# Kernel tuning notes

Measured on AMD Instinct MI355X. Metric: run time of the kernel, lower is better.

The kernel has to match this reference:

```python
import jax, jax.numpy as jnp
import numpy as np

N_EPOCH = 1000
LR = 1e-3      # torch.optim.Adam defaults
BETA1 = 0.9
BETA2 = 0.999
EPS = 1e-8


def setup_inputs() -> dict:
    key = jax.random.key(0)
    k1, k2 = jax.random.split(key)
    H = jax.random.normal(k1, (128, 2048), dtype=jnp.float32)        # test activations [n_test, d]
    H_train = jax.random.normal(k2, (2048, 2048), dtype=jnp.float32)  # corpus activations [n_train, d]
    return {"H": H, "H_train": H_train}


def reference(H, H_train):
    n_test, n_train = H.shape[0], H_train.shape[0]

    def loss_fn(P):
        W = jax.nn.softmax(P, axis=-1)              # [n_test, n_train]
        H_approx = W @ H_train                       # einsum ij,jk->ik
        return jnp.sum((H_approx - H) ** 2)

    grad_fn = jax.grad(loss_fn)

    P0 = jnp.zeros((n_test, n_train), dtype=H.dtype)
    m0 = jnp.zeros_like(P0)
    v0 = jnp.zeros_like(P0)

    def adam_step(carry, t):
        P, m, v = carry
        g = grad_fn(P)
        m = BETA1 * m + (1.0 - BETA1) * g
        v = BETA2 * v + (1.0 - BETA2) * (g * g)
        m_hat = m / (1.0 - BETA1 ** t)
        v_hat = v / (1.0 - BETA2 ** t)
        P = P - LR * m_hat / (jnp.sqrt(v_hat) + EPS)
        return (P, m, v), None

    steps = jnp.arange(1, N_EPOCH + 1, dtype=H.dtype)  # 1-based Adam step count
    (P, _, _), _ = jax.lax.scan(adam_step, (P0, m0, v0), steps)
    return jax.nn.softmax(P, axis=-1)
```

## Files before the change

### kernel.cpp

```cpp
#include <hip/hip_runtime.h>
#include <math.h>

#define DN 2048
#define NT 128

#define KS   16
#define KSL  128
#define KCH  32
#define CB   256
#define RB   32

constexpr float LR    = 1e-3f;
constexpr float BETA1 = 0.9f;
constexpr float BETA2 = 0.999f;
constexpr float EPSA  = 1e-8f;

__device__ __forceinline__ float f4get(const float4& v, int k) {
    return k == 0 ? v.x : (k == 1 ? v.y : (k == 2 ? v.z : v.w));
}

__global__ __launch_bounds__(256)
void wa_kernel(const float* __restrict__ W, const float* __restrict__ A,
               float* __restrict__ parts)
{
    __shared__ __align__(16) float At[KCH][CB];
    const int colb  = blockIdx.x * CB;
    const int rowb  = blockIdx.y * RB;
    const int kb    = blockIdx.z;
    const int kbase = kb * KSL;
    const int tx    = threadIdx.x;
    const int lane  = tx & 63;
    const int wid   = __builtin_amdgcn_readfirstlane(tx >> 6);
    const int row0  = rowb + wid * 8;

    const float* wbase = W + (size_t)row0 * DN + kbase;

    float4 acc[8];
    #pragma unroll
    for (int r = 0; r < 8; ++r) acc[r] = {0.f, 0.f, 0.f, 0.f};

    #pragma unroll 1
    for (int ch = 0; ch < KSL / KCH; ++ch) {
        __syncthreads();
        {
            const float* src = A + (size_t)(kbase + ch * KCH) * DN + colb;
            #pragma unroll
            for (int it = 0; it < 8; ++it) {
                const int f  = it * 256 + tx;
                const int kr = f >> 6;
                const int c4 = f & 63;
                *(float4*)&At[kr][c4 * 4] =
                    *(const float4*)&src[(size_t)kr * DN + c4 * 4];
            }
        }
        __syncthreads();

        #pragma unroll
        for (int kc = 0; kc < KCH / 4; ++kc) {
            float4 wv[8];
            #pragma unroll
            for (int r = 0; r < 8; ++r)
                wv[r] = *(const float4*)(wbase + (size_t)r * DN + ch * KCH + kc * 4);
            #pragma unroll
            for (int kk = 0; kk < 4; ++kk) {
                const float4 av = *(const float4*)&At[4 * kc + kk][lane * 4];
                #pragma unroll
                for (int r = 0; r < 8; ++r) {
                    const float wk = f4get(wv[r], kk);
                    acc[r].x += wk * av.x; acc[r].y += wk * av.y;
                    acc[r].z += wk * av.z; acc[r].w += wk * av.w;
                }
            }
        }
    }

    float* op = parts + (size_t)kb * (NT * DN);
    #pragma unroll
    for (int r = 0; r < 8; ++r)
        *(float4*)&op[(size_t)(row0 + r) * DN + colb + lane * 4] = acc[r];
}

__global__ __launch_bounds__(512)
void bpart_kernel(const float* __restrict__ L, const float* __restrict__ R,
                  float* __restrict__ out_parts)
{
    __shared__ __align__(16) float Ws[128][36];
    __shared__ __align__(16) float At[32][36];
    const int j0    = blockIdx.x * 32;
    const int kbase = blockIdx.y * 512;
    const int tx = threadIdx.x;
    const int cg = tx & 7;
    const int rg = tx >> 3;
    float4 acc0 = {0.f, 0.f, 0.f, 0.f};
    float4 acc1 = {0.f, 0.f, 0.f, 0.f};

    for (int s = 0; s < 16; ++s) {
        const int k0 = kbase + s * 32;
        {
            int idx = tx;
            #pragma unroll
            for (int rr = 0; rr < 2; ++rr) {
                const int row = idx >> 3, f = idx & 7;
                const float4 wv = *(const float4*)&L[row * DN + k0 + 4 * f];
                *(float4*)&Ws[row][4 * f] = wv;
                idx += 512;
            }
            if (tx < 256) {
                const int c = tx >> 3, f = tx & 7;
                const float4 av = *(const float4*)&R[(size_t)(j0 + c) * DN + k0 + 4 * f];
                At[4 * f + 0][c] = av.x;
                At[4 * f + 1][c] = av.y;
                At[4 * f + 2][c] = av.z;
                At[4 * f + 3][c] = av.w;
            }
        }
        __syncthreads();
        #pragma unroll
        for (int kq = 0; kq < 8; ++kq) {
            const float4 w0 = *(const float4*)&Ws[rg][4 * kq];
            const float4 w1 = *(const float4*)&Ws[rg + 64][4 * kq];
            #pragma unroll
            for (int kk = 0; kk < 4; ++kk) {
                const float4 av = *(const float4*)&At[4 * kq + kk][4 * cg];
                const float wa = f4get(w0, kk);
                const float wb = f4get(w1, kk);
                acc0.x += wa * av.x; acc0.y += wa * av.y;
                acc0.z += wa * av.z; acc0.w += wa * av.w;
                acc1.x += wb * av.x; acc1.y += wb * av.y;
                acc1.z += wb * av.z; acc1.w += wb * av.w;
            }
        }
        __syncthreads();
    }
    float* op = out_parts + (size_t)blockIdx.y * (NT * DN);
    *(float4*)&op[rg * DN + j0 + 4 * cg] = acc0;
    *(float4*)&op[(rg + 64) * DN + j0 + 4 * cg] = acc1;
}

__global__ __launch_bounds__(256)
void gram_kernel(const float* __restrict__ Ht, float* __restrict__ A)
{
    __shared__ __align__(16) float Ti[64][36];
    __shared__ __align__(16) float Tj[64][36];
    const int i0 = blockIdx.x * 64, j0 = blockIdx.y * 64;
    const int tx = threadIdx.x;
    const int ti = tx & 15;
    const int tj = tx >> 4;
    float4 acc[4];
    #pragma unroll
    for (int a = 0; a < 4; ++a) acc[a] = {0.f, 0.f, 0.f, 0.f};

    for (int s = 0; s < 64; ++s) {
        const int k0 = s * 32;
        {
            int idx = tx;
            #pragma unroll
            for (int rr = 0; rr < 2; ++rr) {
                const int row = idx >> 3, f = idx & 7;
                *(float4*)&Ti[row][4 * f] = *(const float4*)&Ht[(size_t)(i0 + row) * DN + k0 + 4 * f];
                *(float4*)&Tj[row][4 * f] = *(const float4*)&Ht[(size_t)(j0 + row) * DN + k0 + 4 * f];
                idx += 256;
            }
        }
        __syncthreads();
        #pragma unroll
        for (int kq = 0; kq < 8; ++kq) {
            float4 iv[4], jv[4];
            #pragma unroll
            for (int a = 0; a < 4; ++a) iv[a] = *(const float4*)&Ti[ti + 16 * a][4 * kq];
            #pragma unroll
            for (int b = 0; b < 4; ++b) jv[b] = *(const float4*)&Tj[4 * tj + b][4 * kq];
            #pragma unroll
            for (int kk = 0; kk < 4; ++kk) {
                #pragma unroll
                for (int a = 0; a < 4; ++a) {
                    const float wa = f4get(iv[a], kk);
                    acc[a].x += wa * f4get(jv[0], kk);
                    acc[a].y += wa * f4get(jv[1], kk);
                    acc[a].z += wa * f4get(jv[2], kk);
                    acc[a].w += wa * f4get(jv[3], kk);
                }
            }
        }
        __syncthreads();
    }
    #pragma unroll
    for (int a = 0; a < 4; ++a)
        *(float4*)&A[(size_t)(i0 + ti + 16 * a) * DN + j0 + 4 * tj] = acc[a];
}

__global__ void sumB_kernel(const float* __restrict__ parts, float* __restrict__ Bm)
{
    const int idx = (blockIdx.x * 256 + threadIdx.x) * 4;
    float4 a = *(const float4*)&parts[idx];
    const float4 b = *(const float4*)&parts[(size_t)NT * DN + idx];
    const float4 c = *(const float4*)&parts[(size_t)2 * NT * DN + idx];
    const float4 d = *(const float4*)&parts[(size_t)3 * NT * DN + idx];
    a.x += b.x; a.x += c.x; a.x += d.x;
    a.y += b.y; a.y += c.y; a.y += d.y;
    a.z += b.z; a.z += c.z; a.z += d.z;
    a.w += b.w; a.w += c.w; a.w += d.w;
    *(float4*)&Bm[idx] = a;
}

__global__ void init_kernel(float* __restrict__ P, float* __restrict__ M,
                            float* __restrict__ V, float* __restrict__ W)
{
    const int idx = (blockIdx.x * 256 + threadIdx.x) * 4;
    const float4 z = {0.f, 0.f, 0.f, 0.f};
    const float u = 1.f / (float)DN;
    const float4 uu = {u, u, u, u};
    *(float4*)&P[idx] = z;
    *(float4*)&M[idx] = z;
    *(float4*)&V[idx] = z;
    *(float4*)&W[idx] = uu;
}

__device__ __forceinline__ float blk_sum(float x) {
    #pragma unroll
    for (int o = 32; o > 0; o >>= 1) x += __shfl_down(x, o);
    __shared__ float r[8];
    const int tx = threadIdx.x;
    if ((tx & 63) == 0) r[tx >> 6] = x;
    __syncthreads();
    x = ((r[0] + r[1]) + (r[2] + r[3])) + ((r[4] + r[5]) + (r[6] + r[7]));
    __syncthreads();
    return x;
}

__device__ __forceinline__ float blk_max(float x) {
    #pragma unroll
    for (int o = 32; o > 0; o >>= 1) x = fmaxf(x, __shfl_down(x, o));
    __shared__ float r[8];
    const int tx = threadIdx.x;
    if ((tx & 63) == 0) r[tx >> 6] = x;
    __syncthreads();
    x = fmaxf(fmaxf(fmaxf(r[0], r[1]), fmaxf(r[2], r[3])),
              fmaxf(fmaxf(r[4], r[5]), fmaxf(r[6], r[7])));
    __syncthreads();
    return x;
}

__global__ __launch_bounds__(512)
void adam_kernel(const float* __restrict__ parts, const float* __restrict__ Bm,
                 float* __restrict__ W, float* __restrict__ P,
                 float* __restrict__ M, float* __restrict__ V,
                 const float bc1, const float bc2)
{
    const int i = blockIdx.x;
    const int tx = threadIdx.x;
    const int base = i * DN + tx * 4;

    float4 s = {0.f, 0.f, 0.f, 0.f};
    #pragma unroll
    for (int p = 0; p < KS; ++p) {
        const float4 x = *(const float4*)&parts[(size_t)p * (NT * DN) + base];
        s.x += x.x; s.y += x.y; s.z += x.z; s.w += x.w;
    }
    const float4 b = *(const float4*)&Bm[base];
    float G4[4] = { 2.f * (s.x - b.x), 2.f * (s.y - b.y),
                    2.f * (s.z - b.z), 2.f * (s.w - b.w) };

    float W4[4], P4[4], M4[4], V4[4], E4[4];
    *(float4*)&W4[0] = *(const float4*)&W[base];

    float sp = 0.f;
    #pragma unroll
    for (int e = 0; e < 4; ++e) sp += W4[e] * G4[e];
    const float srow = blk_sum(sp);

    *(float4*)&P4[0] = *(const float4*)&P[base];
    *(float4*)&M4[0] = *(const float4*)&M[base];
    *(float4*)&V4[0] = *(const float4*)&V[base];

    float mx = -1e30f;
    #pragma unroll
    for (int e = 0; e < 4; ++e) {
        const float g  = W4[e] * (G4[e] - srow);
        const float m_ = BETA1 * M4[e] + (1.f - BETA1) * g;
        const float v_ = BETA2 * V4[e] + (1.f - BETA2) * g * g;
        M4[e] = m_; V4[e] = v_;
        const float mh = m_ * bc1;
        const float vh = v_ * bc2;
        const float pn = P4[e] - LR * mh / (sqrtf(vh) + EPSA);
        P4[e] = pn;
        mx = fmaxf(mx, pn);
    }
    mx = blk_max(mx);

    float es = 0.f;
    #pragma unroll
    for (int e = 0; e < 4; ++e) { E4[e] = expf(P4[e] - mx); es += E4[e]; }
    const float sig = blk_sum(es);
    #pragma unroll
    for (int e = 0; e < 4; ++e) W4[e] = E4[e] / sig;

    *(float4*)&W[base] = *(const float4*)&W4[0];
    *(float4*)&P[base] = *(const float4*)&P4[0];
    *(float4*)&M[base] = *(const float4*)&M4[0];
    *(float4*)&V[base] = *(const float4*)&V4[0];
}

extern "C" void kernel_launch(void* const* d_in, const int* in_sizes, int n_in,
                              void* d_out, int out_size, void* d_ws, size_t ws_size,
                              hipStream_t stream)
{
    const float* H  = (const float*)d_in[0];
    const float* Ht = (const float*)d_in[1];

    float* ws = (float*)d_ws;
    float* A     = ws;
    float* Bm    = A  + (size_t)DN * DN;
    float* P     = Bm + (size_t)NT * DN;
    float* M     = P  + (size_t)NT * DN;
    float* V     = M  + (size_t)NT * DN;
    float* W     = V  + (size_t)NT * DN;
    float* parts = W  + (size_t)NT * DN;

    gram_kernel<<<dim3(32, 32), 256, 0, stream>>>(Ht, A);
    bpart_kernel<<<dim3(64, 4), 512, 0, stream>>>(H, Ht, parts);
    sumB_kernel<<<256, 256, 0, stream>>>(parts, Bm);
    init_kernel<<<256, 256, 0, stream>>>(P, M, V, W);

    double b1t = 1.0, b2t = 1.0;
    for (int t = 1; t <= 1000; ++t) {
        b1t *= 0.9; b2t *= 0.999;
        wa_kernel<<<dim3(DN / CB, NT / RB, KS), 256, 0, stream>>>(W, A, parts);
        const float bc1 = (float)(1.0 / (1.0 - b1t));
        const float bc2 = (float)(1.0 / (1.0 - b2t));
        adam_kernel<<<NT, 512, 0, stream>>>(parts, Bm, W, P, M, V, bc1, bc2);
    }

    hipMemcpyAsync(d_out, W, (size_t)NT * DN * sizeof(float),
                   hipMemcpyDeviceToDevice, stream);
}
```

Measured before the change: 28.14 ms.

## Double-buffer A tile in wa_kernel and retile to 512 threads with 8x2 outputs

Reworks the per-step W·A GEMM kernel so the shared-memory A chunk is double-buffered, with the next chunk prefetched while the current one is consumed, and one barrier per chunk. Tile shape changes to 64 rows x 128 columns with 16-deep K chunks and 512 threads, each thread computing 8x2 outputs instead of 8x4. This is meant to hide global-load latency and raise occupancy. In exchange each thread does less work per W load, so W is re-read more often relative to the FMAs.

```diff
diff --git a/kernel.cpp b/kernel.cpp
--- a/kernel.cpp
+++ b/kernel.cpp
@@ -6,9 +6,9 @@
 
 #define KS   16
 #define KSL  128
-#define KCH  32
-#define CB   256
-#define RB   32
+#define KCH  16
+#define CB   128
+#define RB   64
 
 constexpr float LR    = 1e-3f;
 constexpr float BETA1 = 0.9f;
@@ -19,11 +19,11 @@
     return k == 0 ? v.x : (k == 1 ? v.y : (k == 2 ? v.z : v.w));
 }
 
-__global__ __launch_bounds__(256)
+__global__ __launch_bounds__(512, 4)
 void wa_kernel(const float* __restrict__ W, const float* __restrict__ A,
                float* __restrict__ parts)
 {
-    __shared__ __align__(16) float At[KCH][CB];
+    __shared__ __align__(16) float At[2][KCH][CB];
     const int colb  = blockIdx.x * CB;
     const int rowb  = blockIdx.y * RB;
     const int kb    = blockIdx.z;
@@ -35,26 +35,28 @@
 
     const float* wbase = W + (size_t)row0 * DN + kbase;
 
-    float4 acc[8];
-    #pragma unroll
-    for (int r = 0; r < 8; ++r) acc[r] = {0.f, 0.f, 0.f, 0.f};
+    const int s_kr = tx >> 5;
+    const int s_c4 = tx & 31;
+
+    float2 acc[8];
+    #pragma unroll
+    for (int r = 0; r < 8; ++r) acc[r] = {0.f, 0.f};
+
+    {
+        const float* src = A + (size_t)(kbase + 0 * KCH) * DN + colb;
+        *(float4*)&At[0][s_kr][s_c4 * 4] =
+            *(const float4*)&src[(size_t)s_kr * DN + s_c4 * 4];
+    }
+    __syncthreads();
 
     #pragma unroll 1
     for (int ch = 0; ch < KSL / KCH; ++ch) {
-        __syncthreads();
-        {
-            const float* src = A + (size_t)(kbase + ch * KCH) * DN + colb;
-            #pragma unroll
-            for (int it = 0; it < 8; ++it) {
-                const int f  = it * 256 + tx;
-                const int kr = f >> 6;
-                const int c4 = f & 63;
-                *(float4*)&At[kr][c4 * 4] =
-                    *(const float4*)&src[(size_t)kr * DN + c4 * 4];
-            }
-        }
-        __syncthreads();
-
+        if (ch + 1 < KSL / KCH) {
+            const float* src = A + (size_t)(kbase + (ch + 1) * KCH) * DN + colb;
+            *(float4*)&At[(ch + 1) & 1][s_kr][s_c4 * 4] =
+                *(const float4*)&src[(size_t)s_kr * DN + s_c4 * 4];
+        }
+        const int buf = ch & 1;
         #pragma unroll
         for (int kc = 0; kc < KCH / 4; ++kc) {
             float4 wv[8];
@@ -63,21 +65,22 @@
                 wv[r] = *(const float4*)(wbase + (size_t)r * DN + ch * KCH + kc * 4);
             #pragma unroll
             for (int kk = 0; kk < 4; ++kk) {
-                const float4 av = *(const float4*)&At[4 * kc + kk][lane * 4];
+                const float2 av = *(const float2*)&At[buf][4 * kc + kk][lane * 2];
                 #pragma unroll
                 for (int r = 0; r < 8; ++r) {
                     const float wk = f4get(wv[r], kk);
-                    acc[r].x += wk * av.x; acc[r].y += wk * av.y;
-                    acc[r].z += wk * av.z; acc[r].w += wk * av.w;
+                    acc[r].x += wk * av.x;
+                    acc[r].y += wk * av.y;
                 }
             }
         }
-    }
-
-    float* op = parts + (size_t)kb * (NT * DN);
+        __syncthreads();
+    }
+
+    float* op = parts + (size_t)kb * (NT * DN) + colb + lane * 2;
     #pragma unroll
     for (int r = 0; r < 8; ++r)
-        *(float4*)&op[(size_t)(row0 + r) * DN + colb + lane * 4] = acc[r];
+        *(float2*)&op[(size_t)(row0 + r) * DN] = acc[r];
 }
 
 __global__ __launch_bounds__(512)
@@ -325,7 +328,7 @@
     double b1t = 1.0, b2t = 1.0;
     for (int t = 1; t <= 1000; ++t) {
         b1t *= 0.9; b2t *= 0.999;
-        wa_kernel<<<dim3(DN / CB, NT / RB, KS), 256, 0, stream>>>(W, A, parts);
+        wa_kernel<<<dim3(DN / CB, NT / RB, KS), 512, 0, stream>>>(W, A, parts);
         const float bc1 = (float)(1.0 / (1.0 - b1t));
         const float bc2 = (float)(1.0 / (1.0 - b2t));
         adam_kernel<<<NT, 512, 0, stream>>>(parts, Bm, W, P, M, V, bc1, bc2);
```

New measurement: 30.21 ms. 1.07x slower.

## Retile W·A GEMM with shared-memory W tile, 8x8 register blocking, double buffering

Applied to the files above, without the earlier changes.

Rewrites the per-step W·A product so each block stages both a transposed W tile and an A tile in padded, double-buffered shared memory. Each thread computes an 8x8 output block, which raises arithmetic intensity over the old scheme where every thread read W straight from global memory. The next chunk's loads are overlapped with compute on the current chunk. The split-K factor rises from 16 to 32, which doubles the partial-sum buffer written here and then reduced by the Adam kernel. It also adds a launch-bounds occupancy hint.

```diff
diff --git a/kernel.cpp b/kernel.cpp
--- a/kernel.cpp
+++ b/kernel.cpp
@@ -4,11 +4,11 @@
 #define DN 2048
 #define NT 128
 
-#define KS   16
-#define KSL  128
-#define KCH  32
-#define CB   256
-#define RB   32
+#define KS   32
+#define KSL  64
+#define KC   16
+#define CB   128
+#define PADW 132
 
 constexpr float LR    = 1e-3f;
 constexpr float BETA1 = 0.9f;
@@ -19,72 +19,102 @@
     return k == 0 ? v.x : (k == 1 ? v.y : (k == 2 ? v.z : v.w));
 }
 
-__global__ __launch_bounds__(256)
+__global__ __launch_bounds__(256, 2)
 void wa_kernel(const float* __restrict__ W, const float* __restrict__ A,
                float* __restrict__ parts)
 {
-    __shared__ __align__(16) float At[KCH][CB];
-    const int colb  = blockIdx.x * CB;
-    const int rowb  = blockIdx.y * RB;
-    const int kb    = blockIdx.z;
-    const int kbase = kb * KSL;
-    const int tx    = threadIdx.x;
-    const int lane  = tx & 63;
-    const int wid   = __builtin_amdgcn_readfirstlane(tx >> 6);
-    const int row0  = rowb + wid * 8;
-
-    const float* wbase = W + (size_t)row0 * DN + kbase;
-
-    float4 acc[8];
-    #pragma unroll
-    for (int r = 0; r < 8; ++r) acc[r] = {0.f, 0.f, 0.f, 0.f};
+    __shared__ __align__(16) float Ws[2][KC][PADW];
+    __shared__ __align__(16) float As[2][KC][PADW];
+    const int c0 = blockIdx.x * CB;
+    const int kb = blockIdx.y;
+    const int k0 = kb * KSL;
+    const int tx = threadIdx.x;
+    const int i  = tx >> 4;
+    const int j  = tx & 15;
+
+    const int wf_r = tx & 127;
+    const int af_k = tx >> 5;
+    const int af_c = tx & 31;
+
+    float4 acc[8][2];
+    #pragma unroll
+    for (int m = 0; m < 8; ++m) { acc[m][0] = {0,0,0,0}; acc[m][1] = {0,0,0,0}; }
+
+    {
+        #pragma unroll
+        for (int it = 0; it < 2; ++it) {
+            const int f = it * 256 + tx;
+            const int r = f & 127, q = f >> 7;
+            const float4 v = *(const float4*)&W[(size_t)r * DN + k0 + 4 * q];
+            Ws[0][4 * q + 0][r] = v.x;
+            Ws[0][4 * q + 1][r] = v.y;
+            Ws[0][4 * q + 2][r] = v.z;
+            Ws[0][4 * q + 3][r] = v.w;
+        }
+        #pragma unroll
+        for (int it = 0; it < 2; ++it) {
+            const int k = it * 8 + af_k;
+            *(float4*)&As[0][k][4 * af_c] =
+                *(const float4*)&A[(size_t)(k0 + k) * DN + c0 + 4 * af_c];
+        }
+    }
+    __syncthreads();
 
     #pragma unroll 1
-    for (int ch = 0; ch < KSL / KCH; ++ch) {
-        __syncthreads();
-        {
-            const float* src = A + (size_t)(kbase + ch * KCH) * DN + colb;
-            #pragma unroll
-            for (int it = 0; it < 8; ++it) {
-                const int f  = it * 256 + tx;
-                const int kr = f >> 6;
-                const int c4 = f & 63;
-                *(float4*)&At[kr][c4 * 4] =
-                    *(const float4*)&src[(size_t)kr * DN + c4 * 4];
-            }
-        }
-        __syncthreads();
-
-        #pragma unroll
-        for (int kc = 0; kc < KCH / 4; ++kc) {
-            float4 wv[8];
-            #pragma unroll
-            for (int r = 0; r < 8; ++r)
-                wv[r] = *(const float4*)(wbase + (size_t)r * DN + ch * KCH + kc * 4);
-            #pragma unroll
-            for (int kk = 0; kk < 4; ++kk) {
-                const float4 av = *(const float4*)&At[4 * kc + kk][lane * 4];
-                #pragma unroll
-                for (int r = 0; r < 8; ++r) {
-                    const float wk = f4get(wv[r], kk);
-                    acc[r].x += wk * av.x; acc[r].y += wk * av.y;
-                    acc[r].z += wk * av.z; acc[r].w += wk * av.w;
-                }
-            }
-        }
+    for (int ch = 0; ch < KSL / KC; ++ch) {
+        if (ch + 1 < KSL / KC) {
+            const int kc = k0 + (ch + 1) * KC;
+            const int nb = (ch + 1) & 1;
+            #pragma unroll
+            for (int it = 0; it < 2; ++it) {
+                const int f = it * 256 + tx;
+                const int r = f & 127, q = f >> 7;
+                const float4 v = *(const float4*)&W[(size_t)r * DN + kc + 4 * q];
+                Ws[nb][4 * q + 0][r] = v.x;
+                Ws[nb][4 * q + 1][r] = v.y;
+                Ws[nb][4 * q + 2][r] = v.z;
+                Ws[nb][4 * q + 3][r] = v.w;
+            }
+            #pragma unroll
+            for (int it = 0; it < 2; ++it) {
+                const int k = it * 8 + af_k;
+                *(float4*)&As[nb][k][4 * af_c] =
+                    *(const float4*)&A[(size_t)(kc + k) * DN + c0 + 4 * af_c];
+            }
+        }
+        const int buf = ch & 1;
+        #pragma unroll 8
+        for (int kk = 0; kk < KC; ++kk) {
+            const float4 wf0 = *(const float4*)&Ws[buf][kk][8 * i];
+            const float4 wf1 = *(const float4*)&Ws[buf][kk][8 * i + 4];
+            const float4 af0 = *(const float4*)&As[buf][kk][4 * j];
+            const float4 af1 = *(const float4*)&As[buf][kk][64 + 4 * j];
+            #pragma unroll
+            for (int m = 0; m < 8; ++m) {
+                const float wm = (m < 4) ? f4get(wf0, m) : f4get(wf1, m - 4);
+                acc[m][0].x += wm * af0.x; acc[m][0].y += wm * af0.y;
+                acc[m][0].z += wm * af0.z; acc[m][0].w += wm * af0.w;
+                acc[m][1].x += wm * af1.x; acc[m][1].y += wm * af1.y;
+                acc[m][1].z += wm * af1.z; acc[m][1].w += wm * af1.w;
+            }
+        }
+        __syncthreads();
     }
 
     float* op = parts + (size_t)kb * (NT * DN);
     #pragma unroll
-    for (int r = 0; r < 8; ++r)
-        *(float4*)&op[(size_t)(row0 + r) * DN + colb + lane * 4] = acc[r];
+    for (int m = 0; m < 8; ++m) {
+        const int row = 8 * i + m;
+        *(float4*)&op[(size_t)row * DN + c0 + 4 * j]      = acc[m][0];
+        *(float4*)&op[(size_t)row * DN + c0 + 64 + 4 * j] = acc[m][1];
+    }
 }
 
 __global__ __launch_bounds__(512)
 void bpart_kernel(const float* __restrict__ L, const float* __restrict__ R,
                   float* __restrict__ out_parts)
 {
-    __shared__ __align__(16) float Ws[128][36];
+    __shared__ __align__(16) float Wsh[128][36];
     __shared__ __align__(16) float At[32][36];
     const int j0    = blockIdx.x * 32;
     const int kbase = blockIdx.y * 512;
@@ -102,7 +132,7 @@
             for (int rr = 0; rr < 2; ++rr) {
                 const int row = idx >> 3, f = idx & 7;
                 const float4 wv = *(const float4*)&L[row * DN + k0 + 4 * f];
-                *(float4*)&Ws[row][4 * f] = wv;
+                *(float4*)&Wsh[row][4 * f] = wv;
                 idx += 512;
             }
             if (tx < 256) {
@@ -117,8 +147,8 @@
         __syncthreads();
         #pragma unroll
         for (int kq = 0; kq < 8; ++kq) {
-            const float4 w0 = *(const float4*)&Ws[rg][4 * kq];
-            const float4 w1 = *(const float4*)&Ws[rg + 64][4 * kq];
+            const float4 w0 = *(const float4*)&Wsh[rg][4 * kq];
+            const float4 w1 = *(const float4*)&Wsh[rg + 64][4 * kq];
             #pragma unroll
             for (int kk = 0; kk < 4; ++kk) {
                 const float4 av = *(const float4*)&At[4 * kq + kk][4 * cg];
@@ -325,7 +355,7 @@
     double b1t = 1.0, b2t = 1.0;
     for (int t = 1; t <= 1000; ++t) {
         b1t *= 0.9; b2t *= 0.999;
-        wa_kernel<<<dim3(DN / CB, NT / RB, KS), 256, 0, stream>>>(W, A, parts);
+        wa_kernel<<<dim3(DN / CB, DN / KSL), 256, 0, stream>>>(W, A, parts);
         const float bc1 = (float)(1.0 / (1.0 - b1t));
         const float bc2 = (float)(1.0 / (1.0 - b2t));
         adam_kernel<<<NT, 512, 0, stream>>>(parts, Bm, W, P, M, V, bc1, bc2);
```

Result: slower. 29.95 ms (+6.4%).
